# Kernel optimization log

Measured on AMD Instinct MI355X. Metric: run time of the kernel, lower is better.

## Reference

```python
import jax, jax.numpy as jnp
import numpy as np

# Dims: B=batch, N_IN=input capsules, D_IN=input capsule dim,
#       J=output capsules (nb_capsules), C=output capsule dim (capsule_size)
B, N_IN, D_IN, J, C = 32, 2048, 16, 64, 32
ITERS = 5
EPS = 1e-7  # K.epsilon()


def squash(v):
    # Keras code: vector += eps; norm = sum(v^2, -1, keepdims); v * norm/(1+norm)/sqrt(norm)
    v = v + EPS
    n = jnp.sum(v * v, axis=-1, keepdims=True)
    return v * (n / (1.0 + n) / jnp.sqrt(n))


def setup_inputs() -> dict:
    key = jax.random.key(0)
    k1, k2 = jax.random.split(key)
    x = jax.random.normal(k1, (B, N_IN, D_IN, 1), dtype=jnp.float32)
    # glorot_uniform over fan_in=D_IN (last axis), fan_out=C
    limit = float(np.sqrt(6.0 / (D_IN + C)))
    W = jax.random.uniform(k2, (N_IN, J, C, D_IN), dtype=jnp.float32,
                           minval=-limit, maxval=limit)
    return {"x": x, "W": W}


def reference(x, W):
    # x: (B, N_IN, D_IN, 1) -> u: (B, N_IN, D_IN)
    u = x[..., 0]
    # Prediction vectors u_hat[b,i,j] = W[i,j] @ u[b,i] : (B, N_IN, J, C)
    u_hat = jnp.einsum('bid,ijcd->bijc', u, W)
    # Routing logits b_ij: (B, N_IN, J)
    b = jnp.zeros(u_hat.shape[:3], dtype=u_hat.dtype)
    v = None
    for i in range(ITERS):
        c = jax.nn.softmax(b, axis=1)              # softmax over input capsules (axis=1 in source)
        s = jnp.einsum('bij,bijc->bjc', c, u_hat)   # weighted sum over i -> (B, J, C)
        v = squash(s)                                # squash over capsule vector dim C
        if i < ITERS - 1:
            # agreement update: b += <v_j, u_hat_ij>
            b = b + jnp.einsum('bjc,bijc->bij', v, u_hat)
    # match compute_output_shape (B, nb_capsules, capsule_size, 1)
    return v[..., None]
```

## Files before the change

### kernel.cpp

```cpp
#include <hip/hip_runtime.h>
#include <hip/hip_bf16.h>

#define B_ 32
#define N_ 2048
#define D_ 16
#define J_ 64
#define C_ 32
#define NCHUNK 32
#define ICHUNK 64
#define IPW    16

typedef __attribute__((ext_vector_type(8)))  short short8;
typedef __attribute__((ext_vector_type(4)))  short s16x4;
typedef __attribute__((ext_vector_type(16))) float f32x16;
typedef __attribute__((ext_vector_type(4)))  float f32x4;

using bf16_t = __hip_bfloat16;

__global__ __launch_bounds__(256) void prep_u_kernel(const float* __restrict__ x,
                                                     bf16_t* __restrict__ ut) {
  int t  = blockIdx.x * 256 + threadIdx.x;
  int d4 = t & 3;
  int bi = t >> 2;
  int b  = bi & 31;
  int i  = bi >> 5;
  f32x4 xv = *(const f32x4*)(x + ((size_t)(b * N_ + i) * D_ + d4 * 4));
  union { s16x4 v; bf16_t h[4]; } o;
  o.h[0] = __float2bfloat16(xv.x);
  o.h[1] = __float2bfloat16(xv.y);
  o.h[2] = __float2bfloat16(xv.z);
  o.h[3] = __float2bfloat16(xv.w);
  *(s16x4*)(ut + (size_t)(i * B_ + b) * D_ + d4 * 4) = o.v;
}

template<int MODE>
__global__ __launch_bounds__(256) void pass_kernel(
    const float*  __restrict__ Wf,
    const bf16_t* __restrict__ Wb,
    bf16_t*       __restrict__ Wbo,
    const bf16_t* __restrict__ ut,
    const float*  __restrict__ V,
    float*        __restrict__ PS,
    float*        __restrict__ PZ)
{
  constexpr bool UNIFORM = (MODE == 0 || MODE == 2);
  constexpr bool READF32 = (MODE != 1);
  constexpr bool STOREB  = (MODE == 0);

  const int tid  = threadIdx.x;
  const int w    = tid >> 6;
  const int lane = tid & 63;
  const int half = lane >> 5;
  const int lc   = lane & 31;

  const int j  = blockIdx.x / NCHUNK;
  const int ch = blockIdx.x % NCHUNK;

  int crow[16];
#pragma unroll
  for (int r = 0; r < 16; ++r) crow[r] = (r & 3) + 4 * half + 8 * (r >> 2);

  float Vreg[16];
  if (!UNIFORM) {
#pragma unroll
    for (int r = 0; r < 16; ++r) Vreg[r] = V[(lc * J_ + j) * C_ + crow[r]];
  }

  float S[16];
#pragma unroll
  for (int r = 0; r < 16; ++r) S[r] = 0.f;
  float zacc = 0.f;

  const int ibase = ch * ICHUNK + w * IPW;
  const int frag_off = lc * D_ + half * 8;

  const f32x16 zeroacc = {0,0,0,0,0,0,0,0,0,0,0,0,0,0,0,0};

  for (int t = 0; t < IPW; ++t) {
    const int i = ibase + t;
    short8 ufrag = *(const short8*)(ut + (size_t)i * (B_ * D_) + frag_off);
    short8 wfrag;
    const size_t tile = ((size_t)i * J_ + j) * (C_ * D_);
    if (READF32) {
      const float* wp = Wf + tile + frag_off;
      f32x4 w0 = *(const f32x4*)(wp);
      f32x4 w1 = *(const f32x4*)(wp + 4);
      union { short8 v; bf16_t h[8]; } cv;
      cv.h[0] = __float2bfloat16(w0.x);
      cv.h[1] = __float2bfloat16(w0.y);
      cv.h[2] = __float2bfloat16(w0.z);
      cv.h[3] = __float2bfloat16(w0.w);
      cv.h[4] = __float2bfloat16(w1.x);
      cv.h[5] = __float2bfloat16(w1.y);
      cv.h[6] = __float2bfloat16(w1.z);
      cv.h[7] = __float2bfloat16(w1.w);
      wfrag = cv.v;
      if (STOREB) *(short8*)(Wbo + tile + frag_off) = wfrag;
    } else {
      wfrag = *(const short8*)(Wb + tile + frag_off);
    }

    f32x16 acc = __builtin_amdgcn_mfma_f32_32x32x16_bf16(wfrag, ufrag, zeroacc, 0, 0, 0);

    if (UNIFORM) {
#pragma unroll
      for (int r = 0; r < 16; ++r) S[r] += acc[r];
    } else {
      float ph = 0.f;
#pragma unroll
      for (int r = 0; r < 16; ++r) ph = fmaf(Vreg[r], acc[r], ph);
      ph += __shfl_xor(ph, 32);
      float e = __expf(ph);
      zacc += e;
#pragma unroll
      for (int r = 0; r < 16; ++r) S[r] = fmaf(e, acc[r], S[r]);
    }
  }

  __shared__ float S_lds[4 * 32 * 33];
  __shared__ float Z_lds[4 * 32];
#pragma unroll
  for (int r = 0; r < 16; ++r)
    S_lds[w * 1056 + lc * 33 + crow[r]] = S[r];
  if (!half)
    Z_lds[w * 32 + lc] = UNIFORM ? (float)IPW : zacc;
  __syncthreads();

  const size_t pbase = (size_t)blockIdx.x * 1024;
  for (int e = tid; e < 1024; e += 256) {
    int b = e >> 5, c = e & 31;
    PS[pbase + e] = S_lds[b * 33 + c] + S_lds[1056 + b * 33 + c] +
                    S_lds[2112 + b * 33 + c] + S_lds[3168 + b * 33 + c];
  }
  if (tid < 32)
    PZ[(size_t)blockIdx.x * 32 + tid] =
        Z_lds[tid] + Z_lds[32 + tid] + Z_lds[64 + tid] + Z_lds[96 + tid];
}

__global__ __launch_bounds__(256) void combine_kernel(
    const float* __restrict__ PS, const float* __restrict__ PZ,
    float* __restrict__ V, float* __restrict__ out, int first, int last)
{
  int t  = blockIdx.x * 256 + threadIdx.x;
  int c  = t & 31;
  int bj = t >> 5;
  int b  = bj >> 6;
  int j  = bj & 63;
  float s = 0.f, zz = 0.f;
#pragma unroll
  for (int ch = 0; ch < NCHUNK; ++ch) {
    s  += PS[(size_t)(j * NCHUNK + ch) * 1024 + b * 32 + c];
    zz += PZ[(j * NCHUNK + ch) * 32 + b];
  }
  float sv = s / zz + 1e-7f;
  float n = sv * sv;
  n += __shfl_xor(n, 1);
  n += __shfl_xor(n, 2);
  n += __shfl_xor(n, 4);
  n += __shfl_xor(n, 8);
  n += __shfl_xor(n, 16);
  float f = n / ((1.f + n) * sqrtf(n));
  float v = sv * f;
  float Vn = first ? v : (V[t] + v);
  V[t] = Vn;
  if (last) out[t] = v;
}

extern "C" void kernel_launch(void* const* d_in, const int* in_sizes, int n_in,
                              void* d_out, int out_size, void* d_ws, size_t ws_size,
                              hipStream_t stream)
{
  const float* x  = (const float*)d_in[0];
  const float* Wf = (const float*)d_in[1];
  float* out = (float*)d_out;
  char* ws = (char*)d_ws;

  const size_t SZ_WB = (size_t)N_ * J_ * C_ * D_ * 2;
  const size_t SZ_UT = (size_t)N_ * B_ * D_ * 2;
  const size_t SZ_V  = (size_t)B_ * J_ * C_ * 4;
  const size_t SZ_PS = (size_t)J_ * NCHUNK * B_ * C_ * 4;
  const size_t SZ_PZ = (size_t)J_ * NCHUNK * B_ * 4;

  const bool big = ws_size >= SZ_WB + SZ_UT + SZ_V + SZ_PS + SZ_PZ;
  size_t off = big ? SZ_WB : 0;
  bf16_t* Wb = (bf16_t*)ws;
  bf16_t* ut = (bf16_t*)(ws + off); off += SZ_UT;
  float*  V  = (float*)(ws + off);  off += SZ_V;
  float*  PS = (float*)(ws + off);  off += SZ_PS;
  float*  PZ = (float*)(ws + off);

  prep_u_kernel<<<dim3((N_ * B_ * 4) / 256), dim3(256), 0, stream>>>(x, ut);

  dim3 gA(J_ * NCHUNK), blk(256), gB((B_ * J_ * C_) / 256);
  if (big) {
    pass_kernel<0><<<gA, blk, 0, stream>>>(Wf, nullptr, Wb, ut, nullptr, PS, PZ);
    combine_kernel<<<gB, blk, 0, stream>>>(PS, PZ, V, out, 1, 0);
    for (int it = 1; it < 5; ++it) {
      pass_kernel<1><<<gA, blk, 0, stream>>>(nullptr, Wb, nullptr, ut, V, PS, PZ);
      combine_kernel<<<gB, blk, 0, stream>>>(PS, PZ, V, out, 0, it == 4 ? 1 : 0);
    }
  } else {
    pass_kernel<2><<<gA, blk, 0, stream>>>(Wf, nullptr, nullptr, ut, nullptr, PS, PZ);
    combine_kernel<<<gB, blk, 0, stream>>>(PS, PZ, V, out, 1, 0);
    for (int it = 1; it < 5; ++it) {
      pass_kernel<3><<<gA, blk, 0, stream>>>(Wf, nullptr, nullptr, ut, V, PS, PZ);
      combine_kernel<<<gB, blk, 0, stream>>>(PS, PZ, V, out, 0, it == 4 ? 1 : 0);
    }
  }
}
```

Baseline: 510.6 us.

## Fuse combine step into pass kernel via last-block atomic counter

Removes the separate combine kernel: each pass block bumps a per-j atomic counter after writing its partials, and the last block for that j reduces all chunks, applies squash and updates V or the output. The counters are zeroed in the prep kernel. The change also adds nontemporal loads for the fp32 W read, one-step register prefetch of the bf16 W fragment, and skips the Z partials in uniform passes (uses N directly). This saves five kernel launches and their gaps, but serialises the final reduction onto one block per j and adds threadfence and atomic overhead.

```diff
diff --git a/kernel.cpp b/kernel.cpp
--- a/kernel.cpp
+++ b/kernel.cpp
@@ -9,6 +9,7 @@
 #define NCHUNK 32
 #define ICHUNK 64
 #define IPW    16
+#define NPASS  5
 
 typedef __attribute__((ext_vector_type(8)))  short short8;
 typedef __attribute__((ext_vector_type(4)))  short s16x4;
@@ -18,8 +19,10 @@
 using bf16_t = __hip_bfloat16;
 
 __global__ __launch_bounds__(256) void prep_u_kernel(const float* __restrict__ x,
-                                                     bf16_t* __restrict__ ut) {
+                                                     bf16_t* __restrict__ ut,
+                                                     unsigned* __restrict__ counters) {
   int t  = blockIdx.x * 256 + threadIdx.x;
+  if (t < NPASS * J_) counters[t] = 0u;
   int d4 = t & 3;
   int bi = t >> 2;
   int b  = bi & 31;
@@ -41,7 +44,11 @@
     const bf16_t* __restrict__ ut,
     const float*  __restrict__ V,
     float*        __restrict__ PS,
-    float*        __restrict__ PZ)
+    float*        __restrict__ PZ,
+    float*        __restrict__ Vout,
+    float*        __restrict__ out,
+    unsigned*     __restrict__ counter,
+    int first, int last)
 {
   constexpr bool UNIFORM = (MODE == 0 || MODE == 2);
   constexpr bool READF32 = (MODE != 1);
@@ -73,18 +80,18 @@
 
   const int ibase = ch * ICHUNK + w * IPW;
   const int frag_off = lc * D_ + half * 8;
+  const size_t wstride = (size_t)J_ * C_ * D_;
 
   const f32x16 zeroacc = {0,0,0,0,0,0,0,0,0,0,0,0,0,0,0,0};
 
-  for (int t = 0; t < IPW; ++t) {
-    const int i = ibase + t;
-    short8 ufrag = *(const short8*)(ut + (size_t)i * (B_ * D_) + frag_off);
-    short8 wfrag;
-    const size_t tile = ((size_t)i * J_ + j) * (C_ * D_);
-    if (READF32) {
-      const float* wp = Wf + tile + frag_off;
-      f32x4 w0 = *(const f32x4*)(wp);
-      f32x4 w1 = *(const f32x4*)(wp + 4);
+  if (READF32) {
+    const float* wp0 = Wf + ((size_t)ibase * J_ + j) * (C_ * D_) + frag_off;
+    for (int t = 0; t < IPW; ++t) {
+      const int i = ibase + t;
+      short8 ufrag = *(const short8*)(ut + (size_t)i * (B_ * D_) + frag_off);
+      const float* wp = wp0 + (size_t)t * wstride;
+      f32x4 w0 = __builtin_nontemporal_load((const f32x4*)wp);
+      f32x4 w1 = __builtin_nontemporal_load((const f32x4*)(wp + 4));
       union { short8 v; bf16_t h[8]; } cv;
       cv.h[0] = __float2bfloat16(w0.x);
       cv.h[1] = __float2bfloat16(w0.y);
@@ -94,18 +101,35 @@
       cv.h[5] = __float2bfloat16(w1.y);
       cv.h[6] = __float2bfloat16(w1.z);
       cv.h[7] = __float2bfloat16(w1.w);
-      wfrag = cv.v;
-      if (STOREB) *(short8*)(Wbo + tile + frag_off) = wfrag;
-    } else {
-      wfrag = *(const short8*)(Wb + tile + frag_off);
+      short8 wfrag = cv.v;
+      if (STOREB) *(short8*)(Wbo + (size_t)i * wstride + j * (C_ * D_) + frag_off) = wfrag;
+
+      f32x16 acc = __builtin_amdgcn_mfma_f32_32x32x16_bf16(wfrag, ufrag, zeroacc, 0, 0, 0);
+      if (UNIFORM) {
+#pragma unroll
+        for (int r = 0; r < 16; ++r) S[r] += acc[r];
+      } else {
+        float ph = 0.f;
+#pragma unroll
+        for (int r = 0; r < 16; ++r) ph = fmaf(Vreg[r], acc[r], ph);
+        ph += __shfl_xor(ph, 32);
+        float e = __expf(ph);
+        zacc += e;
+#pragma unroll
+        for (int r = 0; r < 16; ++r) S[r] = fmaf(e, acc[r], S[r]);
+      }
     }
-
-    f32x16 acc = __builtin_amdgcn_mfma_f32_32x32x16_bf16(wfrag, ufrag, zeroacc, 0, 0, 0);
-
-    if (UNIFORM) {
-#pragma unroll
-      for (int r = 0; r < 16; ++r) S[r] += acc[r];
-    } else {
+  } else {
+    const bf16_t* wp0 = Wb + ((size_t)ibase * J_ + j) * (C_ * D_) + frag_off;
+    short8 wnext = *(const short8*)wp0;
+    for (int t = 0; t < IPW; ++t) {
+      const int i = ibase + t;
+      short8 wfrag = wnext;
+      if (t + 1 < IPW)
+        wnext = *(const short8*)(wp0 + (size_t)(t + 1) * wstride);
+      short8 ufrag = *(const short8*)(ut + (size_t)i * (B_ * D_) + frag_off);
+
+      f32x16 acc = __builtin_amdgcn_mfma_f32_32x32x16_bf16(wfrag, ufrag, zeroacc, 0, 0, 0);
       float ph = 0.f;
 #pragma unroll
       for (int r = 0; r < 16; ++r) ph = fmaf(Vreg[r], acc[r], ph);
@@ -122,8 +146,8 @@
 #pragma unroll
   for (int r = 0; r < 16; ++r)
     S_lds[w * 1056 + lc * 33 + crow[r]] = S[r];
-  if (!half)
-    Z_lds[w * 32 + lc] = UNIFORM ? (float)IPW : zacc;
+  if (!UNIFORM && !half)
+    Z_lds[w * 32 + lc] = zacc;
   __syncthreads();
 
   const size_t pbase = (size_t)blockIdx.x * 1024;
@@ -132,38 +156,40 @@
     PS[pbase + e] = S_lds[b * 33 + c] + S_lds[1056 + b * 33 + c] +
                     S_lds[2112 + b * 33 + c] + S_lds[3168 + b * 33 + c];
   }
-  if (tid < 32)
+  if (!UNIFORM && tid < 32)
     PZ[(size_t)blockIdx.x * 32 + tid] =
         Z_lds[tid] + Z_lds[32 + tid] + Z_lds[64 + tid] + Z_lds[96 + tid];
-}
-
-__global__ __launch_bounds__(256) void combine_kernel(
-    const float* __restrict__ PS, const float* __restrict__ PZ,
-    float* __restrict__ V, float* __restrict__ out, int first, int last)
-{
-  int t  = blockIdx.x * 256 + threadIdx.x;
-  int c  = t & 31;
-  int bj = t >> 5;
-  int b  = bj >> 6;
-  int j  = bj & 63;
-  float s = 0.f, zz = 0.f;
-#pragma unroll
-  for (int ch = 0; ch < NCHUNK; ++ch) {
-    s  += PS[(size_t)(j * NCHUNK + ch) * 1024 + b * 32 + c];
-    zz += PZ[(j * NCHUNK + ch) * 32 + b];
-  }
-  float sv = s / zz + 1e-7f;
-  float n = sv * sv;
-  n += __shfl_xor(n, 1);
-  n += __shfl_xor(n, 2);
-  n += __shfl_xor(n, 4);
-  n += __shfl_xor(n, 8);
-  n += __shfl_xor(n, 16);
-  float f = n / ((1.f + n) * sqrtf(n));
-  float v = sv * f;
-  float Vn = first ? v : (V[t] + v);
-  V[t] = Vn;
-  if (last) out[t] = v;
+
+  __threadfence();
+  __shared__ int lastflag;
+  if (tid == 0)
+    lastflag = (atomicAdd(counter + j, 1u) == NCHUNK - 1);
+  __syncthreads();
+  if (!lastflag) return;
+  __threadfence();
+
+  for (int e = tid; e < 1024; e += 256) {
+    int b = e >> 5, c = e & 31;
+    float s = 0.f, zz = 0.f;
+#pragma unroll
+    for (int q = 0; q < NCHUNK; ++q) {
+      s += PS[(size_t)(j * NCHUNK + q) * 1024 + e];
+      if (!UNIFORM) zz += PZ[(j * NCHUNK + q) * 32 + b];
+    }
+    if (UNIFORM) zz = (float)N_;
+    float sv = s / zz + 1e-7f;
+    float n = sv * sv;
+    n += __shfl_xor(n, 1);
+    n += __shfl_xor(n, 2);
+    n += __shfl_xor(n, 4);
+    n += __shfl_xor(n, 8);
+    n += __shfl_xor(n, 16);
+    float f = n / ((1.f + n) * sqrtf(n));
+    float v = sv * f;
+    int idx = (b * J_ + j) * C_ + c;
+    if (last) out[idx] = v;
+    else      Vout[idx] = first ? v : (V[idx] + v);
+  }
 }
 
 extern "C" void kernel_launch(void* const* d_in, const int* in_sizes, int n_in,
@@ -180,31 +206,33 @@
   const size_t SZ_V  = (size_t)B_ * J_ * C_ * 4;
   const size_t SZ_PS = (size_t)J_ * NCHUNK * B_ * C_ * 4;
   const size_t SZ_PZ = (size_t)J_ * NCHUNK * B_ * 4;
-
-  const bool big = ws_size >= SZ_WB + SZ_UT + SZ_V + SZ_PS + SZ_PZ;
+  const size_t SZ_CN = (size_t)NPASS * J_ * 4;
+
+  const bool big = ws_size >= SZ_WB + SZ_UT + SZ_V + SZ_PS + SZ_PZ + SZ_CN;
   size_t off = big ? SZ_WB : 0;
   bf16_t* Wb = (bf16_t*)ws;
   bf16_t* ut = (bf16_t*)(ws + off); off += SZ_UT;
   float*  V  = (float*)(ws + off);  off += SZ_V;
   float*  PS = (float*)(ws + off);  off += SZ_PS;
-  float*  PZ = (float*)(ws + off);
-
-  prep_u_kernel<<<dim3((N_ * B_ * 4) / 256), dim3(256), 0, stream>>>(x, ut);
-
-  dim3 gA(J_ * NCHUNK), blk(256), gB((B_ * J_ * C_) / 256);
+  float*  PZ = (float*)(ws + off);  off += SZ_PZ;
+  unsigned* cnt = (unsigned*)(ws + off);
+
+  prep_u_kernel<<<dim3((N_ * B_ * 4) / 256), dim3(256), 0, stream>>>(x, ut, cnt);
+
+  dim3 gA(J_ * NCHUNK), blk(256);
   if (big) {
-    pass_kernel<0><<<gA, blk, 0, stream>>>(Wf, nullptr, Wb, ut, nullptr, PS, PZ);
-    combine_kernel<<<gB, blk, 0, stream>>>(PS, PZ, V, out, 1, 0);
-    for (int it = 1; it < 5; ++it) {
-      pass_kernel<1><<<gA, blk, 0, stream>>>(nullptr, Wb, nullptr, ut, V, PS, PZ);
-      combine_kernel<<<gB, blk, 0, stream>>>(PS, PZ, V, out, 0, it == 4 ? 1 : 0);
-    }
+    pass_kernel<0><<<gA, blk, 0, stream>>>(Wf, nullptr, Wb, ut, nullptr,
+                                           PS, PZ, V, out, cnt + 0 * J_, 1, 0);
+    for (int it = 1; it < 5; ++it)
+      pass_kernel<1><<<gA, blk, 0, stream>>>(nullptr, Wb, nullptr, ut, V,
+                                             PS, PZ, V, out, cnt + it * J_,
+                                             0, it == 4 ? 1 : 0);
   } else {
-    pass_kernel<2><<<gA, blk, 0, stream>>>(Wf, nullptr, nullptr, ut, nullptr, PS, PZ);
-    combine_kernel<<<gB, blk, 0, stream>>>(PS, PZ, V, out, 1, 0);
-    for (int it = 1; it < 5; ++it) {
-      pass_kernel<3><<<gA, blk, 0, stream>>>(Wf, nullptr, nullptr, ut, V, PS, PZ);
-      combine_kernel<<<gB, blk, 0, stream>>>(PS, PZ, V, out, 0, it == 4 ? 1 : 0);
-    }
+    pass_kernel<2><<<gA, blk, 0, stream>>>(Wf, nullptr, nullptr, ut, nullptr,
+                                           PS, PZ, V, out, cnt + 0 * J_, 1, 0);
+    for (int it = 1; it < 5; ++it)
+      pass_kernel<3><<<gA, blk, 0, stream>>>(Wf, nullptr, nullptr, ut, V,
+                                             PS, PZ, V, out, cnt + it * J_,
+                                             0, it == 4 ? 1 : 0);
   }
 }
```

Measured after the change: 2.016 ms. +294.9%, slower.

## Store bf16 W copy in chunk-contiguous layout, prefetch next fragment, nontemporal fp32 loads

Applied to the files above, without the earlier changes.

The bf16 copy of W written in the first pass is re-laid out so that each wave's 16 input capsules for a given output capsule j are contiguous, instead of strided by J*C*D. Later routing passes can then stream W sequentially. The later passes also software-prefetch the next W fragment one iteration ahead. The first pass reads fp32 W with nontemporal loads to reduce cache pollution. This adds register pressure and relies on the producer and consumer agreeing on the new layout.

```diff
diff --git a/kernel.cpp b/kernel.cpp
--- a/kernel.cpp
+++ b/kernel.cpp
@@ -73,18 +73,19 @@
 
   const int ibase = ch * ICHUNK + w * IPW;
   const int frag_off = lc * D_ + half * 8;
+  const size_t wstride  = (size_t)J_ * C_ * D_;
+  const size_t wbbase = ((size_t)(ch * J_ + j) * ICHUNK + w * IPW) * (C_ * D_);
 
   const f32x16 zeroacc = {0,0,0,0,0,0,0,0,0,0,0,0,0,0,0,0};
 
-  for (int t = 0; t < IPW; ++t) {
-    const int i = ibase + t;
-    short8 ufrag = *(const short8*)(ut + (size_t)i * (B_ * D_) + frag_off);
-    short8 wfrag;
-    const size_t tile = ((size_t)i * J_ + j) * (C_ * D_);
-    if (READF32) {
-      const float* wp = Wf + tile + frag_off;
-      f32x4 w0 = *(const f32x4*)(wp);
-      f32x4 w1 = *(const f32x4*)(wp + 4);
+  if (READF32) {
+    const float* wp0 = Wf + ((size_t)ibase * J_ + j) * (C_ * D_) + frag_off;
+    for (int t = 0; t < IPW; ++t) {
+      const int i = ibase + t;
+      short8 ufrag = *(const short8*)(ut + (size_t)i * (B_ * D_) + frag_off);
+      const float* wp = wp0 + (size_t)t * wstride;
+      f32x4 w0 = __builtin_nontemporal_load((const f32x4*)wp);
+      f32x4 w1 = __builtin_nontemporal_load((const f32x4*)(wp + 4));
       union { short8 v; bf16_t h[8]; } cv;
       cv.h[0] = __float2bfloat16(w0.x);
       cv.h[1] = __float2bfloat16(w0.y);
@@ -94,18 +95,36 @@
       cv.h[5] = __float2bfloat16(w1.y);
       cv.h[6] = __float2bfloat16(w1.z);
       cv.h[7] = __float2bfloat16(w1.w);
-      wfrag = cv.v;
-      if (STOREB) *(short8*)(Wbo + tile + frag_off) = wfrag;
-    } else {
-      wfrag = *(const short8*)(Wb + tile + frag_off);
-    }
-
-    f32x16 acc = __builtin_amdgcn_mfma_f32_32x32x16_bf16(wfrag, ufrag, zeroacc, 0, 0, 0);
-
-    if (UNIFORM) {
-#pragma unroll
-      for (int r = 0; r < 16; ++r) S[r] += acc[r];
-    } else {
+      short8 wfrag = cv.v;
+      if (STOREB)
+        *(short8*)(Wbo + wbbase + (size_t)t * (C_ * D_) + frag_off) = wfrag;
+
+      f32x16 acc = __builtin_amdgcn_mfma_f32_32x32x16_bf16(wfrag, ufrag, zeroacc, 0, 0, 0);
+      if (UNIFORM) {
+#pragma unroll
+        for (int r = 0; r < 16; ++r) S[r] += acc[r];
+      } else {
+        float ph = 0.f;
+#pragma unroll
+        for (int r = 0; r < 16; ++r) ph = fmaf(Vreg[r], acc[r], ph);
+        ph += __shfl_xor(ph, 32);
+        float e = __expf(ph);
+        zacc += e;
+#pragma unroll
+        for (int r = 0; r < 16; ++r) S[r] = fmaf(e, acc[r], S[r]);
+      }
+    }
+  } else {
+    const bf16_t* wp0 = Wb + wbbase + frag_off;
+    short8 wnext = *(const short8*)wp0;
+    for (int t = 0; t < IPW; ++t) {
+      const int i = ibase + t;
+      short8 wfrag = wnext;
+      if (t + 1 < IPW)
+        wnext = *(const short8*)(wp0 + (size_t)(t + 1) * (C_ * D_));
+      short8 ufrag = *(const short8*)(ut + (size_t)i * (B_ * D_) + frag_off);
+
+      f32x16 acc = __builtin_amdgcn_mfma_f32_32x32x16_bf16(wfrag, ufrag, zeroacc, 0, 0, 0);
       float ph = 0.f;
 #pragma unroll
       for (int r = 0; r < 16; ++r) ph = fmaf(Vreg[r], acc[r], ph);
```

Result: slower. 540.7 us (+5.9%).
